# Optimization experiments

Hardware: AMD Instinct MI355X
Metric: run time of the kernel (lower is better)

The kernel has to match this reference:

```python
import jax, jax.numpy as jnp
import numpy as np

SIGMA = 5.0
KSIZE = 31  # int(6*sigma+1), odd
CHANNEL = 3

def build_gaussian_kernel(size, sigma):
    coords = jnp.arange(size, dtype=jnp.float32) - size // 2
    g = jnp.exp(-coords ** 2 / (2.0 * sigma ** 2))
    g = g / g.sum()
    k2d = g[:, None] * g[None, :]            # (k, k)
    # depthwise kernel: (O=C, I/g=1, k, k)
    return jnp.broadcast_to(k2d[None, None], (CHANNEL, 1, size, size))

def depthwise_blur(x, kernel):
    # x: (B, C, H, W); kernel: (C, 1, k, k); groups = C, SAME-style padding k//2
    pad = KSIZE // 2
    return jax.lax.conv_general_dilated(
        x, kernel,
        window_strides=(1, 1),
        padding=((pad, pad), (pad, pad)),
        dimension_numbers=("NCHW", "OIHW", "NCHW"),
        feature_group_count=CHANNEL,
    )

def setup_inputs() -> dict:
    key = jax.random.key(0)
    k1, k2 = jax.random.split(key)
    B, C, H, W = 16, 3, 512, 512
    background = jax.random.uniform(k1, (B, C, H, W), dtype=jnp.float32)
    insatance = jax.random.uniform(k2, (B, C, H, W), dtype=jnp.float32)
    gaussian_kernel = build_gaussian_kernel(KSIZE, SIGMA)
    return {"background": background, "insatance": insatance,
            "gaussian_kernel": gaussian_kernel}

def reference(background, insatance, gaussian_kernel):
    # retinex_decompose(background): only illumination1 is used downstream
    bg_log = jnp.log1p(background)
    illumination1 = depthwise_blur(bg_log, gaussian_kernel)
    # retinex_decompose(insatance): reflectance2 = log1p(ins) - blur(log1p(ins))
    ins_log = jnp.log1p(insatance)
    illumination2 = depthwise_blur(ins_log, gaussian_kernel)
    reflectance2 = ins_log - illumination2
    # adjust_illumination(reflectance2, illumination1)
    img_log = reflectance2 + illumination1
    img_corrected = jnp.clip(jnp.expm1(img_log), 0.0, 1.0)
    return img_corrected
```

## Files before the change

kernel.cpp:

```cpp
#include <hip/hip_runtime.h>


constexpr int W_ = 512, H_ = 512, NIMG = 48;
constexpr int SPITCH = 100;
constexpr int RPITCH = 68;

__device__ constexpr float G[31] = {
    8.8805851e-04f, 1.5861066e-03f, 2.7217699e-03f, 4.4874399e-03f,
    7.1084368e-03f, 1.0818767e-02f, 1.5820117e-02f, 2.2226435e-02f,
    3.0002549e-02f, 3.8911209e-02f, 4.8486352e-02f, 5.8048702e-02f,
    6.6771901e-02f, 7.3794364e-02f, 7.8357552e-02f, 7.9940480e-02f,
    7.8357552e-02f, 7.3794364e-02f, 6.6771901e-02f, 5.8048702e-02f,
    4.8486352e-02f, 3.8911209e-02f, 3.0002549e-02f, 2.2226435e-02f,
    1.5820117e-02f, 1.0818767e-02f, 7.1084368e-03f, 4.4874399e-03f,
    2.7217699e-03f, 1.5861066e-03f, 8.8805851e-04f};

__global__ __launch_bounds__(256, 3) void retinex_roll(const float* __restrict__ bg,
                                                       const float* __restrict__ ins,
                                                       float* __restrict__ out) {
  __shared__ __align__(16) float sd[32 * SPITCH];
  __shared__ __align__(16) float hr[64 * RPITCH];

  const int tid  = threadIdx.x;
  const int lane = tid & 63;
  const int x0 = blockIdx.x * 64;
  const int y0 = blockIdx.y * 256;
  const size_t base = (size_t)blockIdx.z * (size_t)(H_ * W_);

  int sr[3], sc[3], gx[3]; bool okx[3];
#pragma unroll
  for (int s = 0; s < 3; ++s) {
    const int item = tid + 256 * s;
    sr[s] = item / 24;
    sc[s] = item - 24 * sr[s];
    gx[s] = x0 - 16 + 4 * sc[s];
    okx[s] = (unsigned)gx[s] < (unsigned)W_;
  }
  const int hrow = tid >> 3;
  const int hcg  = tid & 7;
  const int eg = __builtin_amdgcn_readfirstlane(tid >> 6);

  float4 pb[3], pn[3];
#pragma unroll
  for (int s = 0; s < 3; ++s) {
    const int gy = y0 - 15 + sr[s];
    pb[s] = make_float4(0.f, 0.f, 0.f, 0.f);
    pn[s] = pb[s];
    if (okx[s] && (unsigned)gy < (unsigned)H_) {
      const size_t a = base + (size_t)gy * W_ + gx[s];
      pb[s] = *(const float4*)(bg + a);
      pn[s] = *(const float4*)(ins + a);
    }
  }

#pragma unroll 1
  for (int k = 0; k < 9; ++k) {
#pragma unroll
    for (int s = 0; s < 3; ++s) {
      float4 v;
      v.x = __logf(1.f + pb[s].x) - __logf(1.f + pn[s].x);
      v.y = __logf(1.f + pb[s].y) - __logf(1.f + pn[s].y);
      v.z = __logf(1.f + pb[s].z) - __logf(1.f + pn[s].z);
      v.w = __logf(1.f + pb[s].w) - __logf(1.f + pn[s].w);
      *(float4*)(sd + sr[s] * SPITCH + 4 * sc[s]) = v;
    }
    if (k < 8) {
#pragma unroll
      for (int s = 0; s < 3; ++s) {
        const int gy = y0 + 32 * (k + 1) - 15 + sr[s];
        float4 b0 = make_float4(0.f, 0.f, 0.f, 0.f), n0 = b0;
        if (okx[s] && (unsigned)gy < (unsigned)H_) {
          const size_t a = base + (size_t)gy * W_ + gx[s];
          b0 = *(const float4*)(bg + a);
          n0 = *(const float4*)(ins + a);
        }
        pb[s] = b0; pn[s] = n0;
      }
    }
    __syncthreads();

    {
      float o[8];
#pragma unroll
      for (int e = 0; e < 8; ++e) o[e] = 0.f;
      const float4* p4 = (const float4*)(sd + hrow * SPITCH) + 2 * hcg;
#pragma unroll
      for (int q = 0; q < 10; ++q) {
        const float4 v = p4[q];
        const float w[4] = {v.x, v.y, v.z, v.w};
#pragma unroll
        for (int t = 0; t < 4; ++t) {
          const int pos = 4 * q + t;
#pragma unroll
          for (int e = 0; e < 8; ++e) {
            const int c = pos - 1 - e;
            if (c >= 0 && c < 31) o[e] += G[c] * w[t];
          }
        }
      }
      const int slot = (32 * k - 15 + hrow + 128) & 63;
      float* dst = hr + slot * RPITCH + 8 * hcg;
      *(float4*)(dst)     = make_float4(o[0], o[1], o[2], o[3]);
      *(float4*)(dst + 4) = make_float4(o[4], o[5], o[6], o[7]);
    }
    __syncthreads();

    if (k >= 1) {
      const int t0 = 32 * (k - 1) + 8 * eg;
      float acc[8];
#pragma unroll
      for (int p = 0; p < 8; ++p) acc[p] = 0.f;
#pragma unroll
      for (int j = 0; j < 38; ++j) {
        const int row = (t0 - 15 + j + 128) & 63;
        const float v = hr[row * RPITCH + lane];
#pragma unroll
        for (int p = 0; p < 8; ++p) {
          const int c = j - p;
          if (c >= 0 && c < 31) acc[p] += G[c] * v;
        }
      }
#pragma unroll
      for (int p = 0; p < 8; ++p) {
        const size_t a = base + (size_t)(y0 + t0 + p) * W_ + x0 + lane;
        const float iv = ins[a];
        float r = (1.f + iv) * __expf(acc[p]) - 1.f;
        out[a] = fminf(fmaxf(r, 0.f), 1.f);
      }
    }
  }
}

extern "C" void kernel_launch(void* const* d_in, const int* in_sizes, int n_in,
                              void* d_out, int out_size, void* d_ws, size_t ws_size,
                              hipStream_t stream) {
  const float* bg  = (const float*)d_in[0];
  const float* ins = (const float*)d_in[1];
  float* out = (float*)d_out;
  retinex_roll<<<dim3(8, 2, NIMG), dim3(256), 0, stream>>>(bg, ins, out);
}
```

Before: 162.4 us.

## Software-pipeline blur stages with double-buffered smem to halve barriers per step

```diff
diff --git a/kernel.cpp b/kernel.cpp
--- a/kernel.cpp
+++ b/kernel.cpp
@@ -4,6 +4,7 @@
 constexpr int W_ = 512, H_ = 512, NIMG = 48;
 constexpr int SPITCH = 100;
 constexpr int RPITCH = 68;
+constexpr int RSLOTS = 96;
 
 __device__ constexpr float G[31] = {
     8.8805851e-04f, 1.5861066e-03f, 2.7217699e-03f, 4.4874399e-03f,
@@ -18,8 +19,8 @@
 __global__ __launch_bounds__(256, 3) void retinex_roll(const float* __restrict__ bg,
                                                        const float* __restrict__ ins,
                                                        float* __restrict__ out) {
-  __shared__ __align__(16) float sd[32 * SPITCH];
-  __shared__ __align__(16) float hr[64 * RPITCH];
+  __shared__ __align__(16) float sd[2][32 * SPITCH];
+  __shared__ __align__(16) float hr[RSLOTS * RPITCH];
 
   const int tid  = threadIdx.x;
   const int lane = tid & 63;
@@ -41,6 +42,7 @@
   const int eg = __builtin_amdgcn_readfirstlane(tid >> 6);
 
   float4 pb[3], pn[3];
+
 #pragma unroll
   for (int s = 0; s < 3; ++s) {
     const int gy = y0 - 15 + sr[s];
@@ -52,22 +54,46 @@
       pn[s] = *(const float4*)(ins + a);
     }
   }
+#pragma unroll
+  for (int s = 0; s < 3; ++s) {
+    float4 v;
+    v.x = __logf(1.f + pb[s].x) - __logf(1.f + pn[s].x);
+    v.y = __logf(1.f + pb[s].y) - __logf(1.f + pn[s].y);
+    v.z = __logf(1.f + pb[s].z) - __logf(1.f + pn[s].z);
+    v.w = __logf(1.f + pb[s].w) - __logf(1.f + pn[s].w);
+    *(float4*)(&sd[0][0] + sr[s] * SPITCH + 4 * sc[s]) = v;
+  }
+#pragma unroll
+  for (int s = 0; s < 3; ++s) {
+    const int gy = y0 + 32 - 15 + sr[s];
+    float4 b0 = make_float4(0.f, 0.f, 0.f, 0.f), n0 = b0;
+    if (okx[s] && (unsigned)gy < (unsigned)H_) {
+      const size_t a = base + (size_t)gy * W_ + gx[s];
+      b0 = *(const float4*)(bg + a);
+      n0 = *(const float4*)(ins + a);
+    }
+    pb[s] = b0; pn[s] = n0;
+  }
+  __syncthreads();
 
 #pragma unroll 1
-  for (int k = 0; k < 9; ++k) {
-#pragma unroll
-    for (int s = 0; s < 3; ++s) {
-      float4 v;
-      v.x = __logf(1.f + pb[s].x) - __logf(1.f + pn[s].x);
-      v.y = __logf(1.f + pb[s].y) - __logf(1.f + pn[s].y);
-      v.z = __logf(1.f + pb[s].z) - __logf(1.f + pn[s].z);
-      v.w = __logf(1.f + pb[s].w) - __logf(1.f + pn[s].w);
-      *(float4*)(sd + sr[s] * SPITCH + 4 * sc[s]) = v;
-    }
-    if (k < 8) {
+  for (int k = 0; k < 10; ++k) {
+    if (k <= 7) {
+      float* sb = &sd[(k + 1) & 1][0];
 #pragma unroll
       for (int s = 0; s < 3; ++s) {
-        const int gy = y0 + 32 * (k + 1) - 15 + sr[s];
+        float4 v;
+        v.x = __logf(1.f + pb[s].x) - __logf(1.f + pn[s].x);
+        v.y = __logf(1.f + pb[s].y) - __logf(1.f + pn[s].y);
+        v.z = __logf(1.f + pb[s].z) - __logf(1.f + pn[s].z);
+        v.w = __logf(1.f + pb[s].w) - __logf(1.f + pn[s].w);
+        *(float4*)(sb + sr[s] * SPITCH + 4 * sc[s]) = v;
+      }
+    }
+    if (k <= 6) {
+#pragma unroll
+      for (int s = 0; s < 3; ++s) {
+        const int gy = y0 + 32 * (k + 2) - 15 + sr[s];
         float4 b0 = make_float4(0.f, 0.f, 0.f, 0.f), n0 = b0;
         if (okx[s] && (unsigned)gy < (unsigned)H_) {
           const size_t a = base + (size_t)gy * W_ + gx[s];
@@ -77,13 +103,11 @@
         pb[s] = b0; pn[s] = n0;
       }
     }
-    __syncthreads();
-
-    {
+    if (k <= 8) {
       float o[8];
 #pragma unroll
       for (int e = 0; e < 8; ++e) o[e] = 0.f;
-      const float4* p4 = (const float4*)(sd + hrow * SPITCH) + 2 * hcg;
+      const float4* p4 = (const float4*)(&sd[k & 1][0] + hrow * SPITCH) + 2 * hcg;
 #pragma unroll
       for (int q = 0; q < 10; ++q) {
         const float4 v = p4[q];
@@ -98,21 +122,27 @@
           }
         }
       }
-      const int slot = (32 * k - 15 + hrow + 128) & 63;
+      int bh = 32 * k + 81;
+      bh -= (bh >= 192) ? 192 : 0;
+      bh -= (bh >= 96) ? 96 : 0;
+      int slot = bh + hrow;
+      slot -= (slot >= RSLOTS) ? RSLOTS : 0;
       float* dst = hr + slot * RPITCH + 8 * hcg;
       *(float4*)(dst)     = make_float4(o[0], o[1], o[2], o[3]);
       *(float4*)(dst + 4) = make_float4(o[4], o[5], o[6], o[7]);
     }
-    __syncthreads();
-
-    if (k >= 1) {
-      const int t0 = 32 * (k - 1) + 8 * eg;
+    if (k >= 2) {
+      const int t0 = 32 * (k - 2) + 8 * eg;
+      int be = t0 + 81;
+      be -= (be >= 192) ? 192 : 0;
+      be -= (be >= 96) ? 96 : 0;
       float acc[8];
 #pragma unroll
       for (int p = 0; p < 8; ++p) acc[p] = 0.f;
 #pragma unroll
       for (int j = 0; j < 38; ++j) {
-        const int row = (t0 - 15 + j + 128) & 63;
+        int row = be + j;
+        row -= (row >= RSLOTS) ? RSLOTS : 0;
         const float v = hr[row * RPITCH + lane];
 #pragma unroll
         for (int p = 0; p < 8; ++p) {
@@ -128,6 +158,7 @@
         out[a] = fminf(fmaxf(r, 0.f), 1.f);
       }
     }
+    __syncthreads();
   }
 }
 
```

New measurement: 162.2 us. No clear change (-0.1%).
